# Kernel optimization log

Hardware: AMD Instinct MI355X
Metric: run time of the kernel (lower is better)

Reference implementation:

```python
import jax, jax.numpy as jnp
import numpy as np

B, T, V, E, A, H, IMG, ENC = 128, 25, 10000, 512, 512, 512, 14, 2048
P = IMG * IMG  # 196 pixels


def setup_inputs() -> dict:
    key = jax.random.key(0)
    ks = jax.random.split(key, 24)
    w = lambda i, shape: jax.random.normal(ks[i], shape, jnp.float32) * 0.02
    captions = jax.random.randint(ks[0], (B, T), 0, V, dtype=jnp.int32)
    lens = jax.random.randint(ks[1], (B, 1), 5, T + 1, dtype=jnp.int32)
    lens = lens.at[0, 0].set(T)  # guarantee max(captions_lengths) == T (static)
    encoder_out = jax.random.normal(ks[2], (B, IMG, IMG, ENC), jnp.float32)
    return {
        'captions': captions,
        'encoder_out': encoder_out,
        'captions_lengths': lens,
        'emb_W': w(3, (V, E)),
        'att_enc_W': w(4, (A, ENC)), 'att_enc_b': jnp.zeros((A,), jnp.float32),
        'att_dec_W': w(5, (A, E)), 'att_dec_b': jnp.zeros((A,), jnp.float32),
        'att_fin_W': w(6, (1, A)), 'att_fin_b': jnp.zeros((1,), jnp.float32),
        'f_beta_W': w(7, (ENC, H)), 'f_beta_b': jnp.zeros((ENC,), jnp.float32),
        'W_ih': w(8, (4 * H, ENC + E)), 'b_ih': jnp.zeros((4 * H,), jnp.float32),
        'W_hh': w(9, (4 * H, H)), 'b_hh': jnp.zeros((4 * H,), jnp.float32),
        'lin_W': w(10, (V, H)), 'lin_b': jnp.zeros((V,), jnp.float32),
        'h_init_W': w(11, (H, ENC)), 'h_init_b': jnp.zeros((H,), jnp.float32),
        'c_init_W': w(12, (H, ENC)), 'c_init_b': jnp.zeros((H,), jnp.float32),
    }


def reference(captions, encoder_out, captions_lengths, emb_W,
              att_enc_W, att_enc_b, att_dec_W, att_dec_b, att_fin_W, att_fin_b,
              f_beta_W, f_beta_b, W_ih, b_ih, W_hh, b_hh,
              lin_W, lin_b, h_init_W, h_init_b, c_init_W, c_init_b):
    b = encoder_out.shape[0]
    enc = encoder_out.reshape(b, -1, ENC)                 # [B,P,2048]
    lens = captions_lengths[:, 0]
    sort_ind = jnp.argsort(-lens)                         # descending-length sort
    lens_s = lens[sort_ind]
    enc = enc[sort_ind]
    caps = captions[sort_ind]
    emb = emb_W[caps]                                     # [B,T,E]
    enc_mean = enc.mean(axis=1)                           # [B,2048]
    h0 = enc_mean @ h_init_W.T + h_init_b                 # [B,H]
    c0 = enc_mean @ c_init_W.T + c_init_b
    # precompute encoder side of additive attention (loop-invariant)
    att_enc = jnp.einsum('bpe,ae->bpa', enc, att_enc_W) + att_enc_b  # [B,P,A]

    t_steps = caps.shape[1]
    active = (lens_s[None, :] > jnp.arange(1, t_steps)[:, None])     # [T-1,B]
    emb_prev = jnp.swapaxes(emb[:, :t_steps - 1], 0, 1)              # [T-1,B,E]

    def step(carry, xs):
        h, c = carry
        dec, act = xs                                      # [B,E], [B]
        # additive attention
        att_d = dec @ att_dec_W.T + att_dec_b              # [B,A]
        score = jax.nn.relu(att_enc + att_d[:, None, :]) @ att_fin_W[0] + att_fin_b[0]  # [B,P]
        wts = jax.nn.softmax(score, axis=1)
        ctx = jnp.einsum('bpe,bp->be', enc, wts)           # [B,2048]
        gate = jax.nn.sigmoid(h @ f_beta_W.T + f_beta_b)   # [B,2048]
        ctx = gate * ctx
        x = jnp.concatenate([ctx, dec], axis=1)            # [B,2048+E]
        gates = x @ W_ih.T + b_ih + h @ W_hh.T + b_hh      # [B,4H]
        i, f, g, o = jnp.split(gates, 4, axis=1)
        c_new = jax.nn.sigmoid(f) * c + jax.nn.sigmoid(i) * jnp.tanh(g)
        h_new = jax.nn.sigmoid(o) * jnp.tanh(c_new)
        m = act[:, None]
        h = jnp.where(m, h_new, h)                         # finished rows frozen
        c = jnp.where(m, c_new, c)
        logits = h @ lin_W.T + lin_b                       # [B,V]
        y = jnp.where(m, logits, 0.0)                      # unwritten rows stay 0
        return (h, c), y

    (_, _), ys = jax.lax.scan(step, (h0, c0), (emb_prev, active))
    preds = jnp.zeros((b, t_steps, V), jnp.float32)
    preds = preds.at[:, 0, 0].set(1.0)
    preds = preds.at[:, 1:, :].set(jnp.swapaxes(ys, 0, 1))
    return preds, caps, lens_s, sort_ind
```

## Files before the change

kernel.cpp:

```cpp
#include <hip/hip_runtime.h>
#include <hip/hip_cooperative_groups.h>
#include <math.h>

namespace cg = cooperative_groups;

#define Bb 128
#define Tt 25
#define Vv 10000
#define Ee 512
#define Aa 512
#define Hh 512
#define ENCc 2048
#define Pp 196
#define NSTEP 24
#define NPAD 10112
#define NWG 64

#define OUT_CAPS  ((size_t)Bb*Tt*Vv)
#define OUT_LENS  (OUT_CAPS + (size_t)Bb*Tt)
#define OUT_SORT  (OUT_LENS + Bb)

typedef __bf16 bf16x8 __attribute__((ext_vector_type(8)));
typedef __bf16 bf16x4 __attribute__((ext_vector_type(4)));
typedef float  f32x4  __attribute__((ext_vector_type(4)));

__device__ __forceinline__ float sigm(float x) { return 1.0f / (1.0f + expf(-x)); }

__device__ __forceinline__ void grid_barrier(int* bar)
{
    __syncthreads();
    if (threadIdx.x == 0) {
        __threadfence();
        int g = __hip_atomic_load(bar + 1, __ATOMIC_RELAXED, __HIP_MEMORY_SCOPE_AGENT);
        int a = __hip_atomic_fetch_add(bar, 1, __ATOMIC_ACQ_REL, __HIP_MEMORY_SCOPE_AGENT);
        if (a == NWG - 1) {
            __hip_atomic_store(bar, 0, __ATOMIC_RELAXED, __HIP_MEMORY_SCOPE_AGENT);
            __hip_atomic_store(bar + 1, g + 1, __ATOMIC_RELEASE, __HIP_MEMORY_SCOPE_AGENT);
        } else {
            while (__hip_atomic_load(bar + 1, __ATOMIC_ACQUIRE, __HIP_MEMORY_SCOPE_AGENT) == g)
                __builtin_amdgcn_s_sleep(2);
        }
        __threadfence();
    }
    __syncthreads();
}

__global__ void k_sort(const int* __restrict__ captions, const int* __restrict__ cap_lens,
                       int* sort_ind, int* lens_s, int* caps_s,
                       int* row_emb, int* logit_rowoff, int* logit_mask,
                       float* out)
{
    int b = threadIdx.x;
    __shared__ int lens_sh[Bb];
    int len = cap_lens[b];
    lens_sh[b] = len;
    __syncthreads();
    int r = 0;
    for (int k = 0; k < Bb; k++) {
        int lk = lens_sh[k];
        if (lk > len || (lk == len && k < b)) r++;
    }
    sort_ind[r] = b;
    lens_s[r] = len;
    for (int t = 0; t < Tt; t++) {
        int cv = captions[b * Tt + t];
        caps_s[r * Tt + t] = cv;
        out[OUT_CAPS + (size_t)r * Tt + t] = (float)cv;
    }
    out[OUT_LENS + r] = (float)len;
    out[OUT_SORT + r] = (float)b;
    __syncthreads();
    for (int m = b; m < NSTEP * Bb; m += Bb) {
        int t = m / Bb, bb = m % Bb;
        row_emb[m] = caps_s[bb * Tt + t];
        logit_rowoff[m] = (bb * Tt + (t + 1)) * Vv;
        logit_mask[m] = (lens_s[bb] > t + 1) ? 1 : 0;
    }
}

__global__ void k_preds0(float* out)
{
    size_t i = (size_t)blockIdx.x * 256 + threadIdx.x;
    if (i >= (size_t)Bb * Vv) return;
    size_t b = i / Vv, v = i % Vv;
    out[b * Tt * Vv + v] = (v == 0) ? 1.0f : 0.0f;
}

__global__ void k_bias(const float* b_ih, const float* b_hh,
                       const float* aeb, const float* adb,
                       float* bias2, float* bias_att, int* bar)
{
    int i = blockIdx.x * 256 + threadIdx.x;
    if (i < 2048) bias2[i] = b_ih[i] + b_hh[i];
    if (i < 512)  bias_att[i] = aeb[i] + adb[i];
    if (i < 2)    bar[i] = 0;
}

__global__ void k_cvt_enc(const float* __restrict__ src, const int* __restrict__ sind,
                          __bf16* __restrict__ dst)
{
    int row = blockIdx.y;
    int e4 = blockIdx.x * 256 + threadIdx.x;
    int b = row / Pp, p = row % Pp;
    const float4 v = *(const float4*)(src + ((size_t)(sind[b] * Pp + p)) * ENCc + e4 * 4);
    bf16x4 o = { (__bf16)v.x, (__bf16)v.y, (__bf16)v.z, (__bf16)v.w };
    *(bf16x4*)(dst + (size_t)row * ENCc + e4 * 4) = o;
}

__global__ void k_cvt(const float* __restrict__ src, __bf16* __restrict__ dst, int n4)
{
    int i = blockIdx.x * 256 + threadIdx.x;
    if (i >= n4) return;
    const float4 v = *(const float4*)(src + (size_t)i * 4);
    bf16x4 o = { (__bf16)v.x, (__bf16)v.y, (__bf16)v.z, (__bf16)v.w };
    *(bf16x4*)(dst + (size_t)i * 4) = o;
}

__global__ void k_cvt_lin(const float* __restrict__ src, __bf16* __restrict__ dst)
{
    int i = blockIdx.x * 256 + threadIdx.x;
    if (i >= NPAD * 128) return;
    int row = i >> 7, e = (i & 127) * 4;
    bf16x4 o;
    if (row < Vv) {
        const float4 v = *(const float4*)(src + (size_t)row * Hh + e);
        o = bf16x4{ (__bf16)v.x, (__bf16)v.y, (__bf16)v.z, (__bf16)v.w };
    } else {
        o = bf16x4{ (__bf16)0.f, (__bf16)0.f, (__bf16)0.f, (__bf16)0.f };
    }
    *(bf16x4*)(dst + (size_t)row * Hh + e) = o;
}

__global__ void k_cvt_emb(const float* __restrict__ emb_W, const int* __restrict__ row_emb,
                          __bf16* __restrict__ dst)
{
    int i = blockIdx.x * 256 + threadIdx.x;
    int row = i >> 7, e = (i & 127) * 4;
    const float4 v = *(const float4*)(emb_W + (size_t)row_emb[row] * Ee + e);
    bf16x4 o = { (__bf16)v.x, (__bf16)v.y, (__bf16)v.z, (__bf16)v.w };
    *(bf16x4*)(dst + (size_t)row * Ee + e) = o;
}

__global__ void k_cvt_wihd(const float* __restrict__ W_ih, __bf16* __restrict__ dst)
{
    int i = blockIdx.x * 256 + threadIdx.x;
    int row = i >> 7, e = (i & 127) * 4;
    const float4 v = *(const float4*)(W_ih + (size_t)row * 2560 + 2048 + e);
    bf16x4 o = { (__bf16)v.x, (__bf16)v.y, (__bf16)v.z, (__bf16)v.w };
    *(bf16x4*)(dst + (size_t)row * 512 + e) = o;
}

__global__ void k_wcat2(const float* __restrict__ W_ih, const float* __restrict__ W_hh,
                        __bf16* __restrict__ W2)
{
    int n = blockIdx.y;
    int k4 = blockIdx.x * 256 + threadIdx.x;
    if (k4 >= 640) return;
    int k = k4 * 4;
    float4 v;
    if (k < 2048) v = *(const float4*)(W_ih + (size_t)n * 2560 + k);
    else          v = *(const float4*)(W_hh + (size_t)n * 512 + (k - 2048));
    bf16x4 o = { (__bf16)v.x, (__bf16)v.y, (__bf16)v.z, (__bf16)v.w };
    *(bf16x4*)(W2 + (size_t)n * 2560 + k) = o;
}

__global__ void k_enc_mean(const __bf16* __restrict__ enc, __bf16* __restrict__ emean)
{
    int b = blockIdx.y;
    int e = blockIdx.x * 256 + threadIdx.x;
    const __bf16* base = enc + (size_t)b * Pp * ENCc + e;
    float s = 0.0f;
    for (int p = 0; p < Pp; p++) s += (float)base[(size_t)p * ENCc];
    emean[(size_t)b * ENCc + e] = (__bf16)(s / 196.0f);
}

template<int MODE>
__launch_bounds__(256)
__global__ void mfma_gemm(const __bf16* __restrict__ A, const __bf16* __restrict__ B,
                          const float* __restrict__ bias, void* __restrict__ Cout,
                          int K, int Nout, int Ncol,
                          const int* __restrict__ c_rowoff,
                          const int* __restrict__ mmask,
                          size_t bsA, size_t bsB, size_t bsC)
{
    __shared__ __bf16 sA[128 * 32];
    __shared__ __bf16 sB[128 * 32];
    const int tid = threadIdx.x;
    const int lane = tid & 63;
    const int wave = tid >> 6;
    const int z = blockIdx.z;
    const int m0 = blockIdx.y * 128, n0 = blockIdx.x * 128;
    const int wr = (wave & 1) * 64, wc = (wave >> 1) * 64;
    f32x4 acc[4][4] = {};
    const __bf16* Aptr = A + bsA * z + (size_t)m0 * K;
    const __bf16* Bptr = B + bsB * z + (size_t)n0 * K;
    const int c0 = tid, c1 = tid + 256;
    const int ar0 = c0 >> 2, ak0 = (c0 & 3) * 8;
    const int ar1 = c1 >> 2, ak1 = (c1 & 3) * 8;
    const int kq = (lane >> 4) * 8, mr = lane & 15;

    for (int k0 = 0; k0 < K; k0 += 32) {
        __builtin_amdgcn_global_load_lds(
            (const __attribute__((address_space(1))) void*)(Aptr + (size_t)ar0 * K + k0 + ak0),
            (__attribute__((address_space(3))) void*)(sA + c0 * 8), 16, 0, 0);
        __builtin_amdgcn_global_load_lds(
            (const __attribute__((address_space(1))) void*)(Aptr + (size_t)ar1 * K + k0 + ak1),
            (__attribute__((address_space(3))) void*)(sA + c1 * 8), 16, 0, 0);
        __builtin_amdgcn_global_load_lds(
            (const __attribute__((address_space(1))) void*)(Bptr + (size_t)ar0 * K + k0 + ak0),
            (__attribute__((address_space(3))) void*)(sB + c0 * 8), 16, 0, 0);
        __builtin_amdgcn_global_load_lds(
            (const __attribute__((address_space(1))) void*)(Bptr + (size_t)ar1 * K + k0 + ak1),
            (__attribute__((address_space(3))) void*)(sB + c1 * 8), 16, 0, 0);
        __syncthreads();
        bf16x8 af[4], bfr[4];
        #pragma unroll
        for (int i = 0; i < 4; i++)
            af[i] = *(const bf16x8*)(sA + (wr + i * 16 + mr) * 32 + kq);
        #pragma unroll
        for (int j = 0; j < 4; j++)
            bfr[j] = *(const bf16x8*)(sB + (wc + j * 16 + mr) * 32 + kq);
        #pragma unroll
        for (int i = 0; i < 4; i++)
            #pragma unroll
            for (int j = 0; j < 4; j++)
                acc[i][j] = __builtin_amdgcn_mfma_f32_16x16x32_bf16(af[i], bfr[j], acc[i][j], 0, 0, 0);
        __syncthreads();
    }

    const int rq = (lane >> 4) * 4, cq = lane & 15;
    #pragma unroll
    for (int i = 0; i < 4; i++) {
        #pragma unroll
        for (int j = 0; j < 4; j++) {
            #pragma unroll
            for (int r = 0; r < 4; r++) {
                int row = m0 + wr + i * 16 + rq + r;
                int col = n0 + wc + j * 16 + cq;
                if ((MODE == 1 || MODE == 2) && col >= Ncol) continue;
                float v = acc[i][j][r] + (bias ? bias[col] : 0.0f);
                size_t ro = (c_rowoff ? (size_t)c_rowoff[row] : (size_t)row * Nout) + bsC * z;
                if (MODE == 2) {
                    if (!mmask[row]) v = 0.0f;
                    ((float*)Cout)[ro + col] = v;
                } else if (MODE == 1) {
                    ((__bf16*)Cout)[ro + col] = (__bf16)v;
                } else {
                    ((float*)Cout)[ro + col] = v;
                }
            }
        }
    }
}

__global__ void k_scores(const __bf16* __restrict__ ET, const float* __restrict__ att_d,
                         const float* __restrict__ fin_W, const float* __restrict__ fin_b,
                         float* __restrict__ wts)
{
    __shared__ float Dls[512 * 12];
    const int b = blockIdx.y;
    const int tb = blockIdx.x * 12;
    const int tid = threadIdx.x;
    #pragma unroll
    for (int tt = 0; tt < 12; tt++)
        for (int a = tid; a < 512; a += 256)
            Dls[a * 12 + tt] = att_d[((size_t)(tb + tt) * Bb + b) * Aa + a];
    __syncthreads();
    const int p = tid;
    if (p >= Pp) return;
    float acc[12];
    #pragma unroll
    for (int i = 0; i < 12; i++) acc[i] = 0.0f;
    const __bf16* ep = ET + (size_t)b * Aa * Pp + p;
    for (int a = 0; a < 512; a++) {
        float e = (float)ep[(size_t)a * Pp];
        float fw = fin_W[a];
        const float4* dp = (const float4*)(Dls + a * 12);
        float4 d0 = dp[0], d1 = dp[1], d2 = dp[2];
        acc[0] += fmaxf(e + d0.x, 0.0f) * fw;
        acc[1] += fmaxf(e + d0.y, 0.0f) * fw;
        acc[2] += fmaxf(e + d0.z, 0.0f) * fw;
        acc[3] += fmaxf(e + d0.w, 0.0f) * fw;
        acc[4] += fmaxf(e + d1.x, 0.0f) * fw;
        acc[5] += fmaxf(e + d1.y, 0.0f) * fw;
        acc[6] += fmaxf(e + d1.z, 0.0f) * fw;
        acc[7] += fmaxf(e + d1.w, 0.0f) * fw;
        acc[8] += fmaxf(e + d2.x, 0.0f) * fw;
        acc[9] += fmaxf(e + d2.y, 0.0f) * fw;
        acc[10] += fmaxf(e + d2.z, 0.0f) * fw;
        acc[11] += fmaxf(e + d2.w, 0.0f) * fw;
    }
    float fb = fin_b[0];
    #pragma unroll
    for (int tt = 0; tt < 12; tt++)
        wts[((size_t)(tb + tt) * Bb + b) * Pp + p] = acc[tt] + fb;
}

__global__ void k_softmax(float* scores)
{
    int tb = blockIdx.x;
    float* row = scores + (size_t)tb * Pp;
    int lane = threadIdx.x;
    float v[4];
    float mx = -1e30f;
    #pragma unroll
    for (int i = 0; i < 4; i++) {
        int p = lane + i * 64;
        v[i] = (p < Pp) ? row[p] : -1e30f;
        mx = fmaxf(mx, v[i]);
    }
    #pragma unroll
    for (int off = 32; off > 0; off >>= 1) mx = fmaxf(mx, __shfl_down(mx, off));
    mx = __shfl(mx, 0);
    float s = 0.0f;
    #pragma unroll
    for (int i = 0; i < 4; i++) {
        int p = lane + i * 64;
        v[i] = (p < Pp) ? expf(v[i] - mx) : 0.0f;
        s += v[i];
    }
    #pragma unroll
    for (int off = 32; off > 0; off >>= 1) s += __shfl_down(s, off);
    s = __shfl(s, 0);
    float inv = 1.0f / s;
    #pragma unroll
    for (int i = 0; i < 4; i++) {
        int p = lane + i * 64;
        if (p < Pp) row[p] = v[i] * inv;
    }
}

__global__ void k_ctx(const __bf16* __restrict__ enc, const float* __restrict__ wts,
                      float* __restrict__ ctx_raw)
{
    int b = blockIdx.y;
    int e = blockIdx.x * 256 + threadIdx.x;
    __shared__ float w_s[NSTEP][Pp];
    int tid = threadIdx.x;
    for (int idx = tid; idx < NSTEP * Pp; idx += 256) {
        int t = idx / Pp, p = idx % Pp;
        w_s[t][p] = wts[((size_t)t * Bb + b) * Pp + p];
    }
    __syncthreads();
    const __bf16* base = enc + (size_t)b * Pp * ENCc + e;
    float acc[NSTEP];
    #pragma unroll
    for (int t = 0; t < NSTEP; t++) acc[t] = 0.0f;
    for (int p = 0; p < Pp; p++) {
        float v = (float)base[(size_t)p * ENCc];
        #pragma unroll
        for (int t = 0; t < NSTEP; t++) acc[t] += w_s[t][p] * v;
    }
    for (int t = 0; t < NSTEP; t++)
        ctx_raw[((size_t)t * Bb + b) * ENCc + e] = acc[t];
}

__device__ __forceinline__ bf16x8 lds_frag(const __bf16* s, int row, int g)
{
    int slot = row * 16 + (g ^ (row & 7));
    return *(const bf16x8*)(s + slot * 8);
}

__launch_bounds__(256)
__global__ void k_loop(__bf16* __restrict__ xctx, __bf16* __restrict__ hbuf0,
                       __bf16* __restrict__ hbuf1, float* __restrict__ cbuf,
                       const float* __restrict__ ctx_raw,
                       const __bf16* __restrict__ fbW, const float* __restrict__ fbb,
                       const __bf16* __restrict__ W2, const float* __restrict__ gdec,
                       __bf16* __restrict__ hall, const int* __restrict__ lens,
                       int* __restrict__ bar)
{
    __shared__ __bf16 sA[128 * 128];
    __shared__ __bf16 sB[32 * 128];
    const int tid = threadIdx.x, lane = tid & 63, wave = tid >> 6;
    const int wg = blockIdx.x;
    const int cq = lane & 15, rq4 = (lane >> 4) * 4;
    const int mbase = wave * 32;
    const int kq = lane >> 4;

    for (int t = 0; t < NSTEP; t++) {
        const __bf16* hcur = (t & 1) ? hbuf1 : hbuf0;
        __bf16* hnext = (t & 1) ? hbuf0 : hbuf1;
        {
            const int cb = wg * 32;
            f32x4 acc[2][2] = {};
            for (int k0 = 0; k0 < 512; k0 += 128) {
                #pragma unroll
                for (int i = 0; i < 8; i++) {
                    int flat = tid + 256 * i;
                    int row = flat >> 4, gs = flat & 15;
                    int gsrc = gs ^ (row & 7);
                    __builtin_amdgcn_global_load_lds(
                        (const __attribute__((address_space(1))) void*)(hcur + (size_t)row * 512 + k0 + gsrc * 8),
                        (__attribute__((address_space(3))) void*)(sA + flat * 8), 16, 0, 0);
                }
                #pragma unroll
                for (int i = 0; i < 2; i++) {
                    int flat = tid + 256 * i;
                    int row = flat >> 4, gs = flat & 15;
                    int gsrc = gs ^ (row & 7);
                    __builtin_amdgcn_global_load_lds(
                        (const __attribute__((address_space(1))) void*)(fbW + (size_t)(cb + row) * 512 + k0 + gsrc * 8),
                        (__attribute__((address_space(3))) void*)(sB + flat * 8), 16, 0, 0);
                }
                __syncthreads();
                #pragma unroll
                for (int ks = 0; ks < 4; ks++) {
                    int g = ks * 4 + kq;
                    bf16x8 af[2], bfv[2];
                    #pragma unroll
                    for (int mi = 0; mi < 2; mi++) af[mi] = lds_frag(sA, mbase + mi * 16 + cq, g);
                    #pragma unroll
                    for (int ni = 0; ni < 2; ni++) bfv[ni] = lds_frag(sB, ni * 16 + cq, g);
                    #pragma unroll
                    for (int mi = 0; mi < 2; mi++)
                        #pragma unroll
                        for (int ni = 0; ni < 2; ni++)
                            acc[mi][ni] = __builtin_amdgcn_mfma_f32_16x16x32_bf16(af[mi], bfv[ni], acc[mi][ni], 0, 0, 0);
                }
                __syncthreads();
            }
            const float* cr = ctx_raw + (size_t)t * Bb * ENCc;
            #pragma unroll
            for (int mi = 0; mi < 2; mi++)
                #pragma unroll
                for (int ni = 0; ni < 2; ni++)
                    #pragma unroll
                    for (int r = 0; r < 4; r++) {
                        int row = mbase + mi * 16 + rq4 + r;
                        int col = cb + ni * 16 + cq;
                        float v = acc[mi][ni][r] + fbb[col];
                        float x = sigm(v) * cr[(size_t)row * ENCc + col];
                        xctx[(size_t)row * ENCc + col] = (__bf16)x;
                    }
        }
        grid_barrier(bar);
        {
            const int jb = wg * 8;
            f32x4 acc[2][2] = {};
            for (int k0 = 0; k0 < 2560; k0 += 128) {
                const bool inH = (k0 >= 2048);
                #pragma unroll
                for (int i = 0; i < 8; i++) {
                    int flat = tid + 256 * i;
                    int row = flat >> 4, gs = flat & 15;
                    int gsrc = gs ^ (row & 7);
                    const __bf16* src = inH ? (hcur + (size_t)row * 512 + (k0 - 2048) + gsrc * 8)
                                            : (xctx + (size_t)row * ENCc + k0 + gsrc * 8);
                    __builtin_amdgcn_global_load_lds(
                        (const __attribute__((address_space(1))) void*)src,
                        (__attribute__((address_space(3))) void*)(sA + flat * 8), 16, 0, 0);
                }
                #pragma unroll
                for (int i = 0; i < 2; i++) {
                    int flat = tid + 256 * i;
                    int row = flat >> 4, gs = flat & 15;
                    int gsrc = gs ^ (row & 7);
                    int wrow = (row >> 3) * 512 + jb + (row & 7);
                    __builtin_amdgcn_global_load_lds(
                        (const __attribute__((address_space(1))) void*)(W2 + (size_t)wrow * 2560 + k0 + gsrc * 8),
                        (__attribute__((address_space(3))) void*)(sB + flat * 8), 16, 0, 0);
                }
                __syncthreads();
                #pragma unroll
                for (int ks = 0; ks < 4; ks++) {
                    int g = ks * 4 + kq;
                    bf16x8 af[2], bfv[2];
                    #pragma unroll
                    for (int mi = 0; mi < 2; mi++) af[mi] = lds_frag(sA, mbase + mi * 16 + cq, g);
                    #pragma unroll
                    for (int ni = 0; ni < 2; ni++) bfv[ni] = lds_frag(sB, ni * 16 + cq, g);
                    #pragma unroll
                    for (int mi = 0; mi < 2; mi++)
                        #pragma unroll
                        for (int ni = 0; ni < 2; ni++)
                            acc[mi][ni] = __builtin_amdgcn_mfma_f32_16x16x32_bf16(af[mi], bfv[ni], acc[mi][ni], 0, 0, 0);
                }
                __syncthreads();
            }
            const int j = jb + (cq & 7);
            const int g0 = cq >> 3;
            #pragma unroll
            for (int mi = 0; mi < 2; mi++)
                #pragma unroll
                for (int r = 0; r < 4; r++) {
                    int row = mbase + mi * 16 + rq4 + r;
                    size_t gb = (size_t)(t * Bb + row) * 2048;
                    float a0 = acc[mi][0][r] + gdec[gb + (size_t)g0 * 512 + j];
                    float a1 = acc[mi][1][r] + gdec[gb + (size_t)(2 + g0) * 512 + j];
                    float p0 = __shfl_xor(a0, 8);
                    float p1 = __shfl_xor(a1, 8);
                    float iv, fv, gv, ov;
                    if (cq < 8) { iv = a0; gv = a1; fv = p0; ov = p1; }
                    else        { iv = p0; gv = p1; fv = a0; ov = a1; }
                    float co = cbuf[(size_t)row * 512 + j];
                    float cn = sigm(fv) * co + sigm(iv) * tanhf(gv);
                    float hn = sigm(ov) * tanhf(cn);
                    bool act = lens[row] > (t + 1);
                    __bf16 hold = hcur[(size_t)row * 512 + j];
                    __bf16 hv = act ? (__bf16)hn : hold;
                    if (cq < 8) {
                        if (act) cbuf[(size_t)row * 512 + j] = cn;
                        hnext[(size_t)row * 512 + j] = hv;
                        hall[((size_t)t * Bb + row) * 512 + j] = hv;
                    }
                }
        }
        grid_barrier(bar);
    }
}

extern "C" void kernel_launch(void* const* d_in, const int* in_sizes, int n_in,
                              void* d_out, int out_size, void* d_ws, size_t ws_size,
                              hipStream_t stream)
{
    const int*   captions    = (const int*)d_in[0];
    const float* encoder_out = (const float*)d_in[1];
    const int*   cap_lens    = (const int*)d_in[2];
    const float* emb_W       = (const float*)d_in[3];
    const float* att_enc_W   = (const float*)d_in[4];
    const float* att_enc_b   = (const float*)d_in[5];
    const float* att_dec_W   = (const float*)d_in[6];
    const float* att_dec_b   = (const float*)d_in[7];
    const float* att_fin_W   = (const float*)d_in[8];
    const float* att_fin_b   = (const float*)d_in[9];
    const float* f_beta_W    = (const float*)d_in[10];
    const float* f_beta_b    = (const float*)d_in[11];
    const float* W_ih        = (const float*)d_in[12];
    const float* b_ih        = (const float*)d_in[13];
    const float* W_hh        = (const float*)d_in[14];
    const float* b_hh        = (const float*)d_in[15];
    const float* lin_W       = (const float*)d_in[16];
    const float* lin_b       = (const float*)d_in[17];
    const float* h_init_W    = (const float*)d_in[18];
    const float* h_init_b    = (const float*)d_in[19];
    const float* c_init_W    = (const float*)d_in[20];
    const float* c_init_b    = (const float*)d_in[21];
    float* out = (float*)d_out;

    float* f = (float*)d_ws;
    float* ctx_raw  = f; f += (size_t)NSTEP * Bb * ENCc;
    float* att_d    = f; f += (size_t)NSTEP * Bb * Aa;
    float* wts      = f; f += (size_t)NSTEP * Bb * Pp;
    float* cbuf     = f; f += (size_t)Bb * Hh;
    float* gdec     = f; f += (size_t)NSTEP * Bb * 2048;
    float* bias2    = f; f += 2048;
    float* bias_att = f; f += 512;
    __bf16* bp = (__bf16*)f;
    __bf16* enc_s = bp; bp += (size_t)Bb * Pp * ENCc + 131072;
    __bf16* ET    = bp; bp += (size_t)Bb * Aa * Pp;
    __bf16* attW  = bp; bp += (size_t)Aa * ENCc;
    __bf16* attdW = bp; bp += (size_t)Aa * Ee;
    __bf16* fbW   = bp; bp += (size_t)ENCc * Hh;
    __bf16* hiW   = bp; bp += (size_t)Hh * ENCc;
    __bf16* ciW   = bp; bp += (size_t)Hh * ENCc;
    __bf16* linWb = bp; bp += (size_t)NPAD * Hh;
    __bf16* embg  = bp; bp += (size_t)NSTEP * Bb * Ee;
    __bf16* hall  = bp; bp += (size_t)NSTEP * Bb * Hh;
    __bf16* hbuf0 = bp; bp += (size_t)Bb * Hh;
    __bf16* hbuf1 = bp; bp += (size_t)Bb * Hh;
    __bf16* emean = bp; bp += (size_t)Bb * ENCc;
    __bf16* W2    = bp; bp += (size_t)2048 * 2560;
    __bf16* Wihd  = bp; bp += (size_t)2048 * 512;
    __bf16* xctx  = bp; bp += (size_t)Bb * ENCc;
    int* ip = (int*)bp;
    int* sort_ind     = ip; ip += Bb;
    int* lens_s       = ip; ip += Bb;
    int* caps_s       = ip; ip += Bb * Tt;
    int* row_emb      = ip; ip += NSTEP * Bb;
    int* logit_rowoff = ip; ip += NSTEP * Bb;
    int* logit_mask   = ip; ip += NSTEP * Bb;
    ip = (int*)(((size_t)ip + 255) & ~(size_t)255);
    int* gbar         = ip; ip += 64;

    k_sort<<<1, Bb, 0, stream>>>(captions, cap_lens, sort_ind, lens_s, caps_s,
                                 row_emb, logit_rowoff, logit_mask, out);
    k_preds0<<<(Bb * Vv + 255) / 256, 256, 0, stream>>>(out);
    k_bias<<<8, 256, 0, stream>>>(b_ih, b_hh, att_enc_b, att_dec_b, bias2, bias_att, gbar);
    k_cvt_enc<<<dim3(2, Bb * Pp), 256, 0, stream>>>(encoder_out, sort_ind, enc_s);
    k_cvt<<<(Aa * ENCc / 4 + 255) / 256, 256, 0, stream>>>(att_enc_W, attW, Aa * ENCc / 4);
    k_cvt<<<(Aa * Ee / 4 + 255) / 256, 256, 0, stream>>>(att_dec_W, attdW, Aa * Ee / 4);
    k_cvt<<<(ENCc * Hh / 4 + 255) / 256, 256, 0, stream>>>(f_beta_W, fbW, ENCc * Hh / 4);
    k_cvt<<<(Hh * ENCc / 4 + 255) / 256, 256, 0, stream>>>(h_init_W, hiW, Hh * ENCc / 4);
    k_cvt<<<(Hh * ENCc / 4 + 255) / 256, 256, 0, stream>>>(c_init_W, ciW, Hh * ENCc / 4);
    k_cvt_lin<<<(NPAD * 128 + 255) / 256, 256, 0, stream>>>(lin_W, linWb);
    k_cvt_emb<<<(NSTEP * Bb * 128) / 256, 256, 0, stream>>>(emb_W, row_emb, embg);
    k_cvt_wihd<<<(2048 * 128) / 256, 256, 0, stream>>>(W_ih, Wihd);
    k_wcat2<<<dim3(3, 2048), 256, 0, stream>>>(W_ih, W_hh, W2);
    k_enc_mean<<<dim3(ENCc / 256, Bb), 256, 0, stream>>>(enc_s, emean);
    mfma_gemm<1><<<dim3(4, 1), 256, 0, stream>>>(emean, hiW, h_init_b, hbuf0,
        ENCc, Hh, 512, nullptr, nullptr, 0, 0, 0);
    mfma_gemm<0><<<dim3(4, 1), 256, 0, stream>>>(emean, ciW, c_init_b, cbuf,
        ENCc, Hh, 512, nullptr, nullptr, 0, 0, 0);
    mfma_gemm<1><<<dim3(2, 4, Bb), 256, 0, stream>>>(attW, enc_s, nullptr, ET,
        ENCc, Pp, Pp, nullptr, nullptr, 0, (size_t)Pp * ENCc, (size_t)Aa * Pp);
    mfma_gemm<0><<<dim3(4, NSTEP * Bb / 128), 256, 0, stream>>>(embg, attdW, bias_att, att_d,
        Ee, Aa, 512, nullptr, nullptr, 0, 0, 0);
    mfma_gemm<0><<<dim3(16, NSTEP * Bb / 128), 256, 0, stream>>>(embg, Wihd, bias2, gdec,
        Ee, 2048, 2048, nullptr, nullptr, 0, 0, 0);
    k_scores<<<dim3(2, Bb), 256, 0, stream>>>(ET, att_d, att_fin_W, att_fin_b, wts);
    k_softmax<<<NSTEP * Bb, 64, 0, stream>>>(wts);
    k_ctx<<<dim3(ENCc / 256, Bb), 256, 0, stream>>>(enc_s, wts, ctx_raw);
    {
        void* args[] = { &xctx, &hbuf0, &hbuf1, &cbuf, &ctx_raw, &fbW,
                         (void*)&f_beta_b, &W2, &gdec, &hall, &lens_s, &gbar };
        hipLaunchCooperativeKernel((void*)k_loop, dim3(NWG), dim3(256), args, 0, stream);
    }
    mfma_gemm<2><<<dim3(NPAD / 128, NSTEP * Bb / 128), 256, 0, stream>>>(hall, linWb, lin_b, out,
        Hh, 0, Vv, logit_rowoff, logit_mask, 0, 0, 0);
}
```

Measured before the change: 2.269 ms.

## Triple-buffer LDS tiles in recurrent loop and keep LSTM state in registers

Both GEMM phases of the persistent recurrent kernel now use a three-stage LDS ring. Loads for the next two K-tiles are issued ahead, and explicit vmcnt waits replace the full syncthreads, so global-to-LDS traffic overlaps the MFMA work. The cell state, previous h, lengths, f_beta bias, ctx_raw and gate-decoder inputs are loaded into registers before they are needed, which takes global reads off the epilogue's critical path. The cost is more LDS use and hand-tuned waitcnt counts that depend on how many loads each lane issues, and cbuf is no longer written back.

```diff
diff --git a/kernel.cpp b/kernel.cpp
--- a/kernel.cpp
+++ b/kernel.cpp
@@ -370,57 +370,94 @@
                        __bf16* __restrict__ hall, const int* __restrict__ lens,
                        int* __restrict__ bar)
 {
-    __shared__ __bf16 sA[128 * 128];
-    __shared__ __bf16 sB[32 * 128];
+    __shared__ __bf16 sA[3][128 * 128];
+    __shared__ __bf16 sB[3][32 * 128];
     const int tid = threadIdx.x, lane = tid & 63, wave = tid >> 6;
     const int wg = blockIdx.x;
     const int cq = lane & 15, rq4 = (lane >> 4) * 4;
     const int mbase = wave * 32;
     const int kq = lane >> 4;
+    const int cb = wg * 32;
+    const int jb = wg * 8;
+    const int j = jb + (cq & 7);
+    const int g0 = cq >> 3;
+
+    float fbv[2];
+    #pragma unroll
+    for (int ni = 0; ni < 2; ni++) fbv[ni] = fbb[cb + ni * 16 + cq];
+    int    lenv[2][4];
+    float  creg[2][4];
+    __bf16 hreg[2][4];
+    #pragma unroll
+    for (int mi = 0; mi < 2; mi++)
+        #pragma unroll
+        for (int r = 0; r < 4; r++) {
+            int row = mbase + mi * 16 + rq4 + r;
+            lenv[mi][r] = lens[row];
+            creg[mi][r] = cbuf[(size_t)row * 512 + j];
+            hreg[mi][r] = hbuf0[(size_t)row * 512 + j];
+        }
 
     for (int t = 0; t < NSTEP; t++) {
         const __bf16* hcur = (t & 1) ? hbuf1 : hbuf0;
         __bf16* hnext = (t & 1) ? hbuf0 : hbuf1;
+
         {
-            const int cb = wg * 32;
-            f32x4 acc[2][2] = {};
-            for (int k0 = 0; k0 < 512; k0 += 128) {
+            const float* cr = ctx_raw + (size_t)t * Bb * ENCc;
+            float crv[2][2][4];
+            #pragma unroll
+            for (int mi = 0; mi < 2; mi++)
+                #pragma unroll
+                for (int ni = 0; ni < 2; ni++)
+                    #pragma unroll
+                    for (int r = 0; r < 4; r++)
+                        crv[mi][ni][r] = cr[(size_t)(mbase + mi * 16 + rq4 + r) * ENCc + cb + ni * 16 + cq];
+
+            auto issueA = [&](int kk, int bi) {
+                const int k0 = kk * 128;
                 #pragma unroll
                 for (int i = 0; i < 8; i++) {
                     int flat = tid + 256 * i;
-                    int row = flat >> 4, gs = flat & 15;
-                    int gsrc = gs ^ (row & 7);
+                    int row = flat >> 4, gs = flat & 15, gsrc = gs ^ (row & 7);
                     __builtin_amdgcn_global_load_lds(
                         (const __attribute__((address_space(1))) void*)(hcur + (size_t)row * 512 + k0 + gsrc * 8),
-                        (__attribute__((address_space(3))) void*)(sA + flat * 8), 16, 0, 0);
+                        (__attribute__((address_space(3))) void*)(&sA[bi][flat * 8]), 16, 0, 0);
                 }
                 #pragma unroll
                 for (int i = 0; i < 2; i++) {
                     int flat = tid + 256 * i;
-                    int row = flat >> 4, gs = flat & 15;
-                    int gsrc = gs ^ (row & 7);
+                    int row = flat >> 4, gs = flat & 15, gsrc = gs ^ (row & 7);
                     __builtin_amdgcn_global_load_lds(
                         (const __attribute__((address_space(1))) void*)(fbW + (size_t)(cb + row) * 512 + k0 + gsrc * 8),
-                        (__attribute__((address_space(3))) void*)(sB + flat * 8), 16, 0, 0);
-                }
-                __syncthreads();
+                        (__attribute__((address_space(3))) void*)(&sB[bi][flat * 8]), 16, 0, 0);
+                }
+            };
+            issueA(0, 0);
+            issueA(1, 1);
+            f32x4 acc[2][2] = {};
+            for (int it = 0; it < 4; it++) {
+                const int bi = it % 3;
+                if (it + 2 < 4) issueA(it + 2, (it + 2) % 3);
+                if (it < 2)       asm volatile("s_waitcnt vmcnt(20)" ::: "memory");
+                else if (it == 2) asm volatile("s_waitcnt vmcnt(10)" ::: "memory");
+                else              asm volatile("s_waitcnt vmcnt(0)" ::: "memory");
+                __builtin_amdgcn_s_barrier();
                 #pragma unroll
                 for (int ks = 0; ks < 4; ks++) {
                     int g = ks * 4 + kq;
                     bf16x8 af[2], bfv[2];
                     #pragma unroll
-                    for (int mi = 0; mi < 2; mi++) af[mi] = lds_frag(sA, mbase + mi * 16 + cq, g);
-                    #pragma unroll
-                    for (int ni = 0; ni < 2; ni++) bfv[ni] = lds_frag(sB, ni * 16 + cq, g);
+                    for (int mi = 0; mi < 2; mi++) af[mi] = lds_frag(sA[bi], mbase + mi * 16 + cq, g);
+                    #pragma unroll
+                    for (int ni = 0; ni < 2; ni++) bfv[ni] = lds_frag(sB[bi], ni * 16 + cq, g);
                     #pragma unroll
                     for (int mi = 0; mi < 2; mi++)
                         #pragma unroll
                         for (int ni = 0; ni < 2; ni++)
                             acc[mi][ni] = __builtin_amdgcn_mfma_f32_16x16x32_bf16(af[mi], bfv[ni], acc[mi][ni], 0, 0, 0);
                 }
-                __syncthreads();
+                __builtin_amdgcn_s_barrier();
             }
-            const float* cr = ctx_raw + (size_t)t * Bb * ENCc;
             #pragma unroll
             for (int mi = 0; mi < 2; mi++)
                 #pragma unroll
@@ -429,78 +466,92 @@
                     for (int r = 0; r < 4; r++) {
                         int row = mbase + mi * 16 + rq4 + r;
                         int col = cb + ni * 16 + cq;
-                        float v = acc[mi][ni][r] + fbb[col];
-                        float x = sigm(v) * cr[(size_t)row * ENCc + col];
+                        float v = acc[mi][ni][r] + fbv[ni];
+                        float x = sigm(v) * crv[mi][ni][r];
                         xctx[(size_t)row * ENCc + col] = (__bf16)x;
                     }
         }
         grid_barrier(bar);
+
         {
-            const int jb = wg * 8;
-            f32x4 acc[2][2] = {};
-            for (int k0 = 0; k0 < 2560; k0 += 128) {
+            const float* gd = gdec + (size_t)t * Bb * 2048;
+            float gdv[2][2][4];
+            #pragma unroll
+            for (int mi = 0; mi < 2; mi++)
+                #pragma unroll
+                for (int r = 0; r < 4; r++) {
+                    int row = mbase + mi * 16 + rq4 + r;
+                    gdv[mi][0][r] = gd[(size_t)row * 2048 + (size_t)g0 * 512 + j];
+                    gdv[mi][1][r] = gd[(size_t)row * 2048 + (size_t)(2 + g0) * 512 + j];
+                }
+            auto issueB = [&](int kk, int bi) {
+                const int k0 = kk * 128;
                 const bool inH = (k0 >= 2048);
                 #pragma unroll
                 for (int i = 0; i < 8; i++) {
                     int flat = tid + 256 * i;
-                    int row = flat >> 4, gs = flat & 15;
-                    int gsrc = gs ^ (row & 7);
+                    int row = flat >> 4, gs = flat & 15, gsrc = gs ^ (row & 7);
                     const __bf16* src = inH ? (hcur + (size_t)row * 512 + (k0 - 2048) + gsrc * 8)
                                             : (xctx + (size_t)row * ENCc + k0 + gsrc * 8);
                     __builtin_amdgcn_global_load_lds(
                         (const __attribute__((address_space(1))) void*)src,
-                        (__attribute__((address_space(3))) void*)(sA + flat * 8), 16, 0, 0);
+                        (__attribute__((address_space(3))) void*)(&sA[bi][flat * 8]), 16, 0, 0);
                 }
                 #pragma unroll
                 for (int i = 0; i < 2; i++) {
                     int flat = tid + 256 * i;
-                    int row = flat >> 4, gs = flat & 15;
-                    int gsrc = gs ^ (row & 7);
+                    int row = flat >> 4, gs = flat & 15, gsrc = gs ^ (row & 7);
                     int wrow = (row >> 3) * 512 + jb + (row & 7);
                     __builtin_amdgcn_global_load_lds(
                         (const __attribute__((address_space(1))) void*)(W2 + (size_t)wrow * 2560 + k0 + gsrc * 8),
-                        (__attribute__((address_space(3))) void*)(sB + flat * 8), 16, 0, 0);
-                }
-                __syncthreads();
+                        (__attribute__((address_space(3))) void*)(&sB[bi][flat * 8]), 16, 0, 0);
+                }
+            };
+            issueB(0, 0);
+            issueB(1, 1);
+            f32x4 acc[2][2] = {};
+            for (int it = 0; it < 20; it++) {
+                const int bi = it % 3;
+                if (it + 2 < 20) issueB(it + 2, (it + 2) % 3);
+                if (it < 18)       asm volatile("s_waitcnt vmcnt(20)" ::: "memory");
+                else if (it == 18) asm volatile("s_waitcnt vmcnt(10)" ::: "memory");
+                else               asm volatile("s_waitcnt vmcnt(0)" ::: "memory");
+                __builtin_amdgcn_s_barrier();
                 #pragma unroll
                 for (int ks = 0; ks < 4; ks++) {
                     int g = ks * 4 + kq;
                     bf16x8 af[2], bfv[2];
                     #pragma unroll
-                    for (int mi = 0; mi < 2; mi++) af[mi] = lds_frag(sA, mbase + mi * 16 + cq, g);
-                    #pragma unroll
-                    for (int ni = 0; ni < 2; ni++) bfv[ni] = lds_frag(sB, ni * 16 + cq, g);
+                    for (int mi = 0; mi < 2; mi++) af[mi] = lds_frag(sA[bi], mbase + mi * 16 + cq, g);
+                    #pragma unroll
+                    for (int ni = 0; ni < 2; ni++) bfv[ni] = lds_frag(sB[bi], ni * 16 + cq, g);
                     #pragma unroll
                     for (int mi = 0; mi < 2; mi++)
                         #pragma unroll
                         for (int ni = 0; ni < 2; ni++)
                             acc[mi][ni] = __builtin_amdgcn_mfma_f32_16x16x32_bf16(af[mi], bfv[ni], acc[mi][ni], 0, 0, 0);
                 }
-                __syncthreads();
+                __builtin_amdgcn_s_barrier();
             }
-            const int j = jb + (cq & 7);
-            const int g0 = cq >> 3;
             #pragma unroll
             for (int mi = 0; mi < 2; mi++)
                 #pragma unroll
                 for (int r = 0; r < 4; r++) {
-                    int row = mbase + mi * 16 + rq4 + r;
-                    size_t gb = (size_t)(t * Bb + row) * 2048;
-                    float a0 = acc[mi][0][r] + gdec[gb + (size_t)g0 * 512 + j];
-                    float a1 = acc[mi][1][r] + gdec[gb + (size_t)(2 + g0) * 512 + j];
+                    float a0 = acc[mi][0][r] + gdv[mi][0][r];
+                    float a1 = acc[mi][1][r] + gdv[mi][1][r];
                     float p0 = __shfl_xor(a0, 8);
                     float p1 = __shfl_xor(a1, 8);
                     float iv, fv, gv, ov;
                     if (cq < 8) { iv = a0; gv = a1; fv = p0; ov = p1; }
                     else        { iv = p0; gv = p1; fv = a0; ov = a1; }
-                    float co = cbuf[(size_t)row * 512 + j];
-                    float cn = sigm(fv) * co + sigm(iv) * tanhf(gv);
+                    float cn = sigm(fv) * creg[mi][r] + sigm(iv) * tanhf(gv);
                     float hn = sigm(ov) * tanhf(cn);
-                    bool act = lens[row] > (t + 1);
-                    __bf16 hold = hcur[(size_t)row * 512 + j];
-                    __bf16 hv = act ? (__bf16)hn : hold;
+                    bool act = lenv[mi][r] > (t + 1);
+                    __bf16 hv = act ? (__bf16)hn : hreg[mi][r];
+                    if (act) creg[mi][r] = cn;
+                    hreg[mi][r] = hv;
                     if (cq < 8) {
-                        if (act) cbuf[(size_t)row * 512 + j] = cn;
+                        int row = mbase + mi * 16 + rq4 + r;
                         hnext[(size_t)row * 512 + j] = hv;
                         hall[((size_t)t * Bb + row) * 512 + j] = hv;
                     }
```

New measurement: 2.111 ms. -7.0%, faster.
